# Performance work log

Measured on AMD Instinct MI355X. Metric: run time of the kernel, lower is better.

Reference implementation:

```python
import jax, jax.numpy as jnp
import numpy as np

SAMPLE_RATE = 16000
FREQ_LOW = 200.0
FREQ_HIGH = 1200.0
# deterministic stand-in for random.uniform(freq_low, freq_high): midpoint
FREQUENCY = 0.5 * (FREQ_LOW + FREQ_HIGH)  # 700 Hz
CUTOFF = FREQUENCY / SAMPLE_RATE          # normalized cutoff, as in cutoff_frequency()
Q = 0.70710678  # standard Butterworth-like quality factor for biquad highpass


def _biquad_highpass_coeffs(cutoff, q):
    # standard audio-EQ-cookbook highpass biquad, cutoff normalized to sample rate
    w0 = 2.0 * np.pi * cutoff
    cw, sw = np.cos(w0), np.sin(w0)
    alpha = sw / (2.0 * q)
    b0 = (1.0 + cw) / 2.0
    b1 = -(1.0 + cw)
    b2 = (1.0 + cw) / 2.0
    a0 = 1.0 + alpha
    a1 = -2.0 * cw
    a2 = 1.0 - alpha
    return (np.float32(b0 / a0), np.float32(b1 / a0), np.float32(b2 / a0),
            np.float32(a1 / a0), np.float32(a2 / a0))


def setup_inputs() -> dict:
    key = jax.random.key(0)
    B, C, T = 128, 2, 65536
    audio = jax.random.normal(key, (B, C, T), dtype=jnp.float32)
    return {"audio": audio}


def reference(audio) -> jnp.ndarray:
    b0, b1, b2, a1, a2 = _biquad_highpass_coeffs(CUTOFF, Q)
    x_t = jnp.moveaxis(audio, -1, 0)  # [T, B, C] for scan over time
    zero = jnp.zeros(x_t.shape[1:], dtype=audio.dtype)

    def step(carry, x):
        x1, x2, y1, y2 = carry
        # IIR biquad difference equation
        y = b0 * x + b1 * x1 + b2 * x2 - a1 * y1 - a2 * y2
        return (x, x1, y, y1), y

    _, y_t = jax.lax.scan(step, (zero, zero, zero, zero), x_t)
    return jnp.moveaxis(y_t, 0, -1)  # [B, C, T]
```

## Files before the change

kernel.cpp:

```cpp
#include <hip/hip_runtime.h>
#include <math.h>


#define T_LEN   65536
#define L_CHUNK 128
#define W_WARM  64
#define TS      32
#define BLK     256
#define STRIDE  33
#define CHUNK_SHIFT 9

__global__ __launch_bounds__(BLK, 2)
void hp_biquad_kernel(const float* __restrict__ x, float* __restrict__ y,
                      float b0, float b1, float b2, float a1, float a2)
{
    __shared__ float lds[BLK * STRIDE];
    const int tid = threadIdx.x;
    const int blk = blockIdx.x;

    float x1 = 0.f, x2 = 0.f, y1 = 0.f, y2 = 0.f;

    const int NT = (W_WARM + L_CHUNK) / TS;
    for (int tile = 0; tile < NT; ++tile) {
        #pragma unroll
        for (int p = 0; p < (BLK * TS / 4) / BLK; ++p) {
            int q   = tid + p * BLK;
            int seg = q >> 3;
            int off = (q & 7) << 2;
            int cg  = blk * BLK + seg;
            int pos = cg * L_CHUNK - W_WARM + tile * TS + off;
            int cbase = (cg >> CHUNK_SHIFT) * T_LEN;
            float4 v = make_float4(0.f, 0.f, 0.f, 0.f);
            if (pos >= cbase)
                v = *(const float4*)(x + pos);
            int a = seg * STRIDE + off;
            lds[a] = v.x; lds[a + 1] = v.y; lds[a + 2] = v.z; lds[a + 3] = v.w;
        }
        __syncthreads();

        {
            int base = tid * STRIDE;
            #pragma unroll
            for (int t = 0; t < TS; ++t) {
                float xv = lds[base + t];
                float yv = b0 * xv + b1 * x1 + b2 * x2 - a1 * y1 - a2 * y2;
                lds[base + t] = yv;
                x2 = x1; x1 = xv;
                y2 = y1; y1 = yv;
            }
        }
        __syncthreads();

        if (tile >= W_WARM / TS) {
            #pragma unroll
            for (int p = 0; p < (BLK * TS / 4) / BLK; ++p) {
                int q   = tid + p * BLK;
                int seg = q >> 3;
                int off = (q & 7) << 2;
                int cg  = blk * BLK + seg;
                int pos = cg * L_CHUNK - W_WARM + tile * TS + off;
                int a   = seg * STRIDE + off;
                float4 v = make_float4(lds[a], lds[a + 1], lds[a + 2], lds[a + 3]);
                *(float4*)(y + pos) = v;
            }
        }
        __syncthreads();
    }
}

extern "C" void kernel_launch(void* const* d_in, const int* in_sizes, int n_in,
                              void* d_out, int out_size, void* d_ws, size_t ws_size,
                              hipStream_t stream)
{
    const float* x = (const float*)d_in[0];
    float* y = (float*)d_out;

    const double SR = 16000.0, FLO = 200.0, FHI = 1200.0;
    const double freq   = 0.5 * (FLO + FHI);
    const double cutoff = freq / SR;
    const double q      = 0.70710678;
    const double w0 = 2.0 * M_PI * cutoff;
    const double cw = cos(w0), sw = sin(w0);
    const double alpha = sw / (2.0 * q);
    const double b0 = (1.0 + cw) / 2.0;
    const double b1 = -(1.0 + cw);
    const double b2 = (1.0 + cw) / 2.0;
    const double a0 = 1.0 + alpha;
    const double a1 = -2.0 * cw;
    const double a2 = 1.0 - alpha;
    const float fb0 = (float)(b0 / a0), fb1 = (float)(b1 / a0), fb2 = (float)(b2 / a0);
    const float fa1 = (float)(a1 / a0), fa2 = (float)(a2 / a0);

    const int total  = 128 * 2 * T_LEN;
    const int chunks = total / L_CHUNK;
    const int blocks = chunks / BLK;

    hp_biquad_kernel<<<blocks, BLK, 0, stream>>>(x, y, fb0, fb1, fb2, fa1, fa2);
    (void)in_sizes; (void)n_in; (void)out_size; (void)d_ws; (void)ws_size;
}
```

Before: 136.9 us.

## Use per-wavefront LDS tiles with register prefetch and swizzled float4 layout

Each wavefront now owns a private LDS region and processes 64 chunks, so block-wide __syncthreads barriers become s_waitcnt lgkmcnt fences. The next tile's global loads are issued into registers before the recurrence runs on the current tile, overlapping memory latency with compute. A rotated float4 slot swizzle replaces the padded stride-33 layout, allowing vector LDS accesses. The chunk length is halved to 64 with the same 64-sample warmup, which doubles parallelism but raises the redundant warmup fraction, and occupancy bounds go from 2 to 4 blocks. Skipping barriers is only safe because each wavefront touches only its own LDS region.

```diff
diff --git a/kernel.cpp b/kernel.cpp
--- a/kernel.cpp
+++ b/kernel.cpp
@@ -3,68 +3,100 @@
 
 
 #define T_LEN   65536
-#define L_CHUNK 128
+#define L_CHUNK 64
 #define W_WARM  64
 #define TS      32
 #define BLK     256
-#define STRIDE  33
-#define CHUNK_SHIFT 9
+#define NT      ((W_WARM + L_CHUNK) / TS)
+#define CHUNK_SHIFT 10
+#define ROWS    64
+#define WLDS    (ROWS * TS)
 
-__global__ __launch_bounds__(BLK, 2)
+__device__ __forceinline__ void lds_fence() {
+    asm volatile("s_waitcnt lgkmcnt(0)" ::: "memory");
+}
+
+__device__ __forceinline__ void load_tile(const float* __restrict__ x,
+                                          int cg0, int tile, float4 pf[8],
+                                          int lane)
+{
+    #pragma unroll
+    for (int p = 0; p < 8; ++p) {
+        int q   = lane + (p << 6);
+        int seg = q >> 3;
+        int g   = q & 7;
+        int cg  = cg0 + seg;
+        int pos = cg * L_CHUNK - W_WARM + tile * TS + (g << 2);
+        int cbase = (cg >> CHUNK_SHIFT) * T_LEN;
+        float4 v = make_float4(0.f, 0.f, 0.f, 0.f);
+        if (pos >= cbase)
+            v = *(const float4*)(x + pos);
+        pf[p] = v;
+    }
+}
+
+__global__ __launch_bounds__(BLK, 4)
 void hp_biquad_kernel(const float* __restrict__ x, float* __restrict__ y,
                       float b0, float b1, float b2, float a1, float a2)
 {
-    __shared__ float lds[BLK * STRIDE];
-    const int tid = threadIdx.x;
-    const int blk = blockIdx.x;
+    __shared__ float lds[4 * WLDS];
+    const int tid  = threadIdx.x;
+    const int lane = tid & 63;
+    const int wv   = tid >> 6;
+    float* wlds = lds + wv * WLDS;
+
+    const int cg0 = (blockIdx.x * 4 + wv) * ROWS;
 
     float x1 = 0.f, x2 = 0.f, y1 = 0.f, y2 = 0.f;
+    float4 pf[8];
 
-    const int NT = (W_WARM + L_CHUNK) / TS;
+    load_tile(x, cg0, 0, pf, lane);
+
     for (int tile = 0; tile < NT; ++tile) {
         #pragma unroll
-        for (int p = 0; p < (BLK * TS / 4) / BLK; ++p) {
-            int q   = tid + p * BLK;
-            int seg = q >> 3;
-            int off = (q & 7) << 2;
-            int cg  = blk * BLK + seg;
-            int pos = cg * L_CHUNK - W_WARM + tile * TS + off;
-            int cbase = (cg >> CHUNK_SHIFT) * T_LEN;
-            float4 v = make_float4(0.f, 0.f, 0.f, 0.f);
-            if (pos >= cbase)
-                v = *(const float4*)(x + pos);
-            int a = seg * STRIDE + off;
-            lds[a] = v.x; lds[a + 1] = v.y; lds[a + 2] = v.z; lds[a + 3] = v.w;
+        for (int p = 0; p < 8; ++p) {
+            int q    = lane + (p << 6);
+            int seg  = q >> 3;
+            int g    = q & 7;
+            int slot = ((g + seg) & 7) << 2;
+            *(float4*)&wlds[seg * TS + slot] = pf[p];
         }
-        __syncthreads();
+        lds_fence();
 
-        {
-            int base = tid * STRIDE;
-            #pragma unroll
-            for (int t = 0; t < TS; ++t) {
-                float xv = lds[base + t];
-                float yv = b0 * xv + b1 * x1 + b2 * x2 - a1 * y1 - a2 * y2;
-                lds[base + t] = yv;
-                x2 = x1; x1 = xv;
-                y2 = y1; y1 = yv;
-            }
+        if (tile + 1 < NT)
+            load_tile(x, cg0, tile + 1, pf, lane);
+
+        #pragma unroll
+        for (int g = 0; g < 8; ++g) {
+            int slot = ((g + lane) & 7) << 2;
+            float4 v = *(float4*)&wlds[lane * TS + slot];
+            float yv;
+            yv = b0 * v.x + b1 * x1 + b2 * x2 - a1 * y1 - a2 * y2;
+            x2 = x1; x1 = v.x; y2 = y1; y1 = yv; v.x = yv;
+            yv = b0 * v.y + b1 * x1 + b2 * x2 - a1 * y1 - a2 * y2;
+            x2 = x1; x1 = v.y; y2 = y1; y1 = yv; v.y = yv;
+            yv = b0 * v.z + b1 * x1 + b2 * x2 - a1 * y1 - a2 * y2;
+            x2 = x1; x1 = v.z; y2 = y1; y1 = yv; v.z = yv;
+            yv = b0 * v.w + b1 * x1 + b2 * x2 - a1 * y1 - a2 * y2;
+            x2 = x1; x1 = v.w; y2 = y1; y1 = yv; v.w = yv;
+            *(float4*)&wlds[lane * TS + slot] = v;
         }
-        __syncthreads();
+        lds_fence();
 
         if (tile >= W_WARM / TS) {
             #pragma unroll
-            for (int p = 0; p < (BLK * TS / 4) / BLK; ++p) {
-                int q   = tid + p * BLK;
-                int seg = q >> 3;
-                int off = (q & 7) << 2;
-                int cg  = blk * BLK + seg;
-                int pos = cg * L_CHUNK - W_WARM + tile * TS + off;
-                int a   = seg * STRIDE + off;
-                float4 v = make_float4(lds[a], lds[a + 1], lds[a + 2], lds[a + 3]);
+            for (int p = 0; p < 8; ++p) {
+                int q    = lane + (p << 6);
+                int seg  = q >> 3;
+                int g    = q & 7;
+                int slot = ((g + seg) & 7) << 2;
+                float4 v = *(float4*)&wlds[seg * TS + slot];
+                int cg   = cg0 + seg;
+                int pos  = cg * L_CHUNK - W_WARM + tile * TS + (g << 2);
                 *(float4*)(y + pos) = v;
             }
+            lds_fence();
         }
-        __syncthreads();
     }
 }
 
```

New measurement: 118.6 us. 13.3% less time.
